# Kernel optimization log

Hardware: AMD Instinct MI355X
Metric: run time of the kernel (lower is better)

## Reference

```python
import jax, jax.numpy as jnp
import numpy as np

IN_C = 256
ATTN_C = IN_C // 8
B, H, W = 4, 64, 64


def setup_inputs() -> dict:
    key = jax.random.key(0)
    ks = jax.random.split(key, 8)
    x = jax.random.normal(ks[0], (B, IN_C, W, H), dtype=jnp.float32)
    # 1x1 convs == channel-mixing matmuls: weight [out_c, in_c], bias [out_c]
    sq = 1.0 / np.sqrt(IN_C)
    Wq = jax.random.normal(ks[1], (ATTN_C, IN_C), dtype=jnp.float32) * sq
    bq = jnp.zeros((ATTN_C,), dtype=jnp.float32)
    Wk = jax.random.normal(ks[2], (ATTN_C, IN_C), dtype=jnp.float32) * sq
    bk = jnp.zeros((ATTN_C,), dtype=jnp.float32)
    Wv = jax.random.normal(ks[3], (IN_C, IN_C), dtype=jnp.float32) * sq
    bv = jnp.zeros((IN_C,), dtype=jnp.float32)
    # gamma initialized to zeros in the torch module; use a nonzero value so
    # the attention path contributes to the output/gradients.
    gamma = jnp.full((1,), 0.5, dtype=jnp.float32)
    return {"x": x, "Wq": Wq, "bq": bq, "Wk": Wk, "bk": bk,
            "Wv": Wv, "bv": bv, "gamma": gamma}


def reference(x, Wq, bq, Wk, bk, Wv, bv, gamma):
    bs, c, w, h = x.shape
    n = w * h
    xf = x.reshape(bs, c, n)                                   # [B, C, N]
    q = jnp.einsum('ac,bcn->ban', Wq, xf) + bq[:, None]        # [B, A, N]
    k = jnp.einsum('ac,bcn->ban', Wk, xf) + bk[:, None]        # [B, A, N]
    v = jnp.einsum('oc,bcn->bon', Wv, xf) + bv[:, None]        # [B, C, N]
    # energy = query.transpose(1,2) @ key  -> energy[b,i,j] = sum_a q[b,a,i] k[b,a,j]
    energy = jnp.einsum('bai,baj->bij', q, k)                  # [B, N, N]
    # non-standard: softmax over dim=1 (the query/i axis)
    attn = jax.nn.softmax(energy, axis=1)
    # out = value @ attn.transpose(1,2) -> out[b,c,i] = sum_j v[b,c,j] attn[b,i,j]
    out = jnp.einsum('bcj,bij->bci', v, attn)                  # [B, C, N]
    out = out.reshape(bs, c, w, h)
    return gamma * out + x
```

## Files before the change

### kernel.cpp

```cpp
#include <hip/hip_runtime.h>

#define NBATCH 4
#define CIN 256
#define CATT 32
#define NPIX 4096

static constexpr float LOG2E_F = 1.4426950408889634f;

typedef __attribute__((ext_vector_type(8))) short bf16x8;
typedef __attribute__((ext_vector_type(4))) float f32x4;

__device__ __forceinline__ unsigned short f2bf_rne(float f) {
    unsigned u = __builtin_bit_cast(unsigned, f);
    return (unsigned short)((u + 0x7fffu + ((u >> 16) & 1u)) >> 16);
}
__device__ __forceinline__ float bf2f(unsigned short h) {
    unsigned u = (unsigned)h << 16;
    return __builtin_bit_cast(float, u);
}
__device__ __forceinline__ void split8(const float* p, bf16x8& hi, bf16x8& lo) {
    const float4 a = *reinterpret_cast<const float4*>(p);
    const float4 b = *reinterpret_cast<const float4*>(p + 4);
    const float f[8] = {a.x, a.y, a.z, a.w, b.x, b.y, b.z, b.w};
    #pragma unroll
    for (int e = 0; e < 8; ++e) {
        const unsigned short h = f2bf_rne(f[e]);
        hi[e] = (short)h;
        lo[e] = (short)f2bf_rne(f[e] - bf2f(h));
    }
}
__device__ __forceinline__ bf16x8 cvt8(const float* p) {
    const float4 a = *reinterpret_cast<const float4*>(p);
    const float4 b = *reinterpret_cast<const float4*>(p + 4);
    const float f[8] = {a.x, a.y, a.z, a.w, b.x, b.y, b.z, b.w};
    bf16x8 r;
    #pragma unroll
    for (int e = 0; e < 8; ++e) r[e] = (short)f2bf_rne(f[e]);
    return r;
}

__global__ __launch_bounds__(256, 2)
void transpose_kernel(const float* __restrict__ x, unsigned short* __restrict__ xT)
{
    __shared__ unsigned short sT[64][68];
    const int t = threadIdx.x;
    const int nblk = blockIdx.x * 64;
    const int cblk = blockIdx.y * 64;
    const int b = blockIdx.z;
    const float* xb = x + ((size_t)b * CIN + cblk) * NPIX + nblk;
    const int lc = t >> 2, ln = (t & 3) << 4;
    #pragma unroll
    for (int u = 0; u < 4; ++u) {
        const float4 v = *reinterpret_cast<const float4*>(&xb[(size_t)lc * NPIX + ln + 4 * u]);
        sT[ln + 4 * u + 0][lc] = f2bf_rne(v.x);
        sT[ln + 4 * u + 1][lc] = f2bf_rne(v.y);
        sT[ln + 4 * u + 2][lc] = f2bf_rne(v.z);
        sT[ln + 4 * u + 3][lc] = f2bf_rne(v.w);
    }
    __syncthreads();
    const int rn = t >> 2, cs = (t & 3) << 4;
    const uint2 d0 = *reinterpret_cast<const uint2*>(&sT[rn][cs + 0]);
    const uint2 d1 = *reinterpret_cast<const uint2*>(&sT[rn][cs + 4]);
    const uint2 d2 = *reinterpret_cast<const uint2*>(&sT[rn][cs + 8]);
    const uint2 d3 = *reinterpret_cast<const uint2*>(&sT[rn][cs + 12]);
    unsigned short* dst = xT + ((size_t)b * NPIX + nblk + rn) * CIN + cblk + cs;
    *reinterpret_cast<uint4*>(dst)     = make_uint4(d0.x, d0.y, d1.x, d1.y);
    *reinterpret_cast<uint4*>(dst + 8) = make_uint4(d2.x, d2.y, d3.x, d3.y);
}

__global__ __launch_bounds__(256, 2)
void proj_qk_kernel(const float* __restrict__ Wq, const float* __restrict__ bq,
                    const float* __restrict__ Wk, const float* __restrict__ bk,
                    const unsigned short* __restrict__ xT,
                    unsigned short* __restrict__ qt, unsigned short* __restrict__ kt)
{
    const int t = threadIdx.x, w = t >> 6, l = t & 63, lr = l & 15, lg = l >> 4;
    const int b = blockIdx.y;
    const int n0 = blockIdx.x * 64 + 16 * w;
    const unsigned short* xrow = xT + ((size_t)b * NPIX + n0 + lr) * CIN + lg * 8;
    f32x4 aq[2] = {{0.f,0.f,0.f,0.f},{0.f,0.f,0.f,0.f}};
    f32x4 ak2[2] = {{0.f,0.f,0.f,0.f},{0.f,0.f,0.f,0.f}};
    #pragma unroll
    for (int ks = 0; ks < 8; ++ks) {
        const int ko = ks * 32 + lg * 8;
        const bf16x8 bx = *reinterpret_cast<const bf16x8*>(xrow + ks * 32);
        #pragma unroll
        for (int mt = 0; mt < 2; ++mt) {
            bf16x8 wh, wl;
            split8(&Wq[(size_t)(mt * 16 + lr) * CIN + ko], wh, wl);
            aq[mt] = __builtin_amdgcn_mfma_f32_16x16x32_bf16(wh, bx, aq[mt], 0, 0, 0);
            aq[mt] = __builtin_amdgcn_mfma_f32_16x16x32_bf16(wl, bx, aq[mt], 0, 0, 0);
            split8(&Wk[(size_t)(mt * 16 + lr) * CIN + ko], wh, wl);
            ak2[mt] = __builtin_amdgcn_mfma_f32_16x16x32_bf16(wh, bx, ak2[mt], 0, 0, 0);
            ak2[mt] = __builtin_amdgcn_mfma_f32_16x16x32_bf16(wl, bx, ak2[mt], 0, 0, 0);
        }
    }
    #pragma unroll
    for (int mt = 0; mt < 2; ++mt) {
        const float4 b4q = *reinterpret_cast<const float4*>(&bq[16 * mt + (lg << 2)]);
        const float4 b4k = *reinterpret_cast<const float4*>(&bk[16 * mt + (lg << 2)]);
        ushort4 uq, uk;
        uq.x = f2bf_rne(LOG2E_F * (aq[mt][0] + b4q.x));
        uq.y = f2bf_rne(LOG2E_F * (aq[mt][1] + b4q.y));
        uq.z = f2bf_rne(LOG2E_F * (aq[mt][2] + b4q.z));
        uq.w = f2bf_rne(LOG2E_F * (aq[mt][3] + b4q.w));
        uk.x = f2bf_rne(ak2[mt][0] + b4k.x);
        uk.y = f2bf_rne(ak2[mt][1] + b4k.y);
        uk.z = f2bf_rne(ak2[mt][2] + b4k.z);
        uk.w = f2bf_rne(ak2[mt][3] + b4k.w);
        const size_t base = ((size_t)b * NPIX + n0 + lr) * CATT + 16 * mt + (lg << 2);
        *reinterpret_cast<ushort4*>(&qt[base]) = uq;
        *reinterpret_cast<ushort4*>(&kt[base]) = uk;
    }
}

__global__ __launch_bounds__(256, 2)
void stats_kernel(const unsigned short* __restrict__ qt,
                  const unsigned short* __restrict__ kt, float* __restrict__ rs)
{
    __shared__ float sred[4][16];
    const int n = blockIdx.x;
    const int b = n & 3;
    const int jblk = (n >> 2) * 32;
    const int t = threadIdx.x, w = t >> 6, l = t & 63, lr = l & 15, lg = l >> 4;
    const int jsl = w & 1;
    const int ih = w >> 1;
    const unsigned short* qb = qt + (size_t)b * NPIX * CATT;
    const unsigned short* kb = kt + (size_t)b * NPIX * CATT;

    const bf16x8 kfrag = *reinterpret_cast<const bf16x8*>(
        &kb[(size_t)(jblk + 16 * jsl + lr) * CATT + lg * 8]);
    const f32x4 zero = {0.f, 0.f, 0.f, 0.f};
    const unsigned short* qp = qb + (size_t)(ih * 2048 + lr) * CATT + lg * 8;

    float s0 = 0.f, s1 = 0.f, s2 = 0.f, s3 = 0.f;
    bf16x8 qc0 = *reinterpret_cast<const bf16x8*>(qp);
    bf16x8 qc1 = *reinterpret_cast<const bf16x8*>(qp + 16 * CATT);
    bf16x8 qc2 = *reinterpret_cast<const bf16x8*>(qp + 32 * CATT);
    bf16x8 qc3 = *reinterpret_cast<const bf16x8*>(qp + 48 * CATT);

    for (int ib = 0; ib < 2048; ib += 64) {
        bf16x8 qn0, qn1, qn2, qn3;
        const bool more = (ib + 64) < 2048;
        if (more) {
            const unsigned short* q2 = qp + (size_t)(ib + 64) * CATT;
            qn0 = *reinterpret_cast<const bf16x8*>(q2);
            qn1 = *reinterpret_cast<const bf16x8*>(q2 + 16 * CATT);
            qn2 = *reinterpret_cast<const bf16x8*>(q2 + 32 * CATT);
            qn3 = *reinterpret_cast<const bf16x8*>(q2 + 48 * CATT);
        }
        f32x4 d;
        d = __builtin_amdgcn_mfma_f32_16x16x32_bf16(kfrag, qc0, zero, 0, 0, 0);
        s0 += __builtin_amdgcn_exp2f(d[0]); s1 += __builtin_amdgcn_exp2f(d[1]);
        s2 += __builtin_amdgcn_exp2f(d[2]); s3 += __builtin_amdgcn_exp2f(d[3]);
        d = __builtin_amdgcn_mfma_f32_16x16x32_bf16(kfrag, qc1, zero, 0, 0, 0);
        s0 += __builtin_amdgcn_exp2f(d[0]); s1 += __builtin_amdgcn_exp2f(d[1]);
        s2 += __builtin_amdgcn_exp2f(d[2]); s3 += __builtin_amdgcn_exp2f(d[3]);
        d = __builtin_amdgcn_mfma_f32_16x16x32_bf16(kfrag, qc2, zero, 0, 0, 0);
        s0 += __builtin_amdgcn_exp2f(d[0]); s1 += __builtin_amdgcn_exp2f(d[1]);
        s2 += __builtin_amdgcn_exp2f(d[2]); s3 += __builtin_amdgcn_exp2f(d[3]);
        d = __builtin_amdgcn_mfma_f32_16x16x32_bf16(kfrag, qc3, zero, 0, 0, 0);
        s0 += __builtin_amdgcn_exp2f(d[0]); s1 += __builtin_amdgcn_exp2f(d[1]);
        s2 += __builtin_amdgcn_exp2f(d[2]); s3 += __builtin_amdgcn_exp2f(d[3]);
        if (more) { qc0 = qn0; qc1 = qn1; qc2 = qn2; qc3 = qn3; }
    }
    #pragma unroll
    for (int m = 1; m < 16; m <<= 1) {
        s0 += __shfl_xor(s0, m); s1 += __shfl_xor(s1, m);
        s2 += __shfl_xor(s2, m); s3 += __shfl_xor(s3, m);
    }
    if (lr == 0) {
        sred[w][(lg << 2) + 0] = s0;
        sred[w][(lg << 2) + 1] = s1;
        sred[w][(lg << 2) + 2] = s2;
        sred[w][(lg << 2) + 3] = s3;
    }
    __syncthreads();
    if (t < 32) {
        const int j16 = t & 15, js = t >> 4;
        const float s = sred[js][j16] + sred[js + 2][j16];
        rs[(size_t)b * NPIX + jblk + t] = 1.0f / s;
    }
}

__global__ __launch_bounds__(256, 2)
void proj_v_kernel(const float* __restrict__ Wv, const float* __restrict__ bv,
                   const unsigned short* __restrict__ xT, const float* __restrict__ rs,
                   const float* __restrict__ gamma, unsigned short* __restrict__ vt)
{
    const int t = threadIdx.x, w = t >> 6, l = t & 63, lr = l & 15, lg = l >> 4;
    const int b = blockIdx.y;
    const int n0 = blockIdx.x * 32;
    const int cb = 64 * w;
    const unsigned short* xa = xT + ((size_t)b * NPIX + n0) * CIN;
    f32x4 acc[2][4] = {};
    #pragma unroll
    for (int ks = 0; ks < 8; ++ks) {
        const int ko = ks * 32 + lg * 8;
        bf16x8 af[2];
        #pragma unroll
        for (int mt = 0; mt < 2; ++mt)
            af[mt] = *reinterpret_cast<const bf16x8*>(&xa[(size_t)(16 * mt + lr) * CIN + ko]);
        #pragma unroll
        for (int ct = 0; ct < 4; ++ct) {
            const bf16x8 wf = cvt8(&Wv[(size_t)(cb + 16 * ct + lr) * CIN + ko]);
            #pragma unroll
            for (int mt = 0; mt < 2; ++mt)
                acc[mt][ct] = __builtin_amdgcn_mfma_f32_16x16x32_bf16(af[mt], wf, acc[mt][ct], 0, 0, 0);
        }
    }
    const float gv = gamma[0];
    #pragma unroll
    for (int mt = 0; mt < 2; ++mt) {
        const int nr = n0 + 16 * mt + (lg << 2);
        const float4 rs4 = *reinterpret_cast<const float4*>(&rs[(size_t)b * NPIX + nr]);
        #pragma unroll
        for (int ct = 0; ct < 4; ++ct) {
            const int c = cb + 16 * ct + lr;
            const float bb = bv[c];
            ushort4 u;
            u.x = f2bf_rne(gv * rs4.x * (acc[mt][ct][0] + bb));
            u.y = f2bf_rne(gv * rs4.y * (acc[mt][ct][1] + bb));
            u.z = f2bf_rne(gv * rs4.z * (acc[mt][ct][2] + bb));
            u.w = f2bf_rne(gv * rs4.w * (acc[mt][ct][3] + bb));
            *reinterpret_cast<ushort4*>(&vt[((size_t)b * CIN + c) * NPIX + nr]) = u;
        }
    }
}

__global__ __launch_bounds__(256, 2)
void out_kernel(const unsigned short* __restrict__ qt,
                const unsigned short* __restrict__ kt,
                const unsigned short* __restrict__ vt,
                const float* __restrict__ x, float* __restrict__ out)
{
    __shared__ unsigned short sP[2][64 * 64];
    const int n = blockIdx.x;
    const int b = n & 3;
    const int rest = n >> 2;
    const int ch = rest & 1;
    const int it = rest >> 1;
    const int iblk = it * 64;
    const int cblk = ch * 128;
    const int t = threadIdx.x, w = t >> 6, l = t & 63, lr = l & 15, lg = l >> 4;
    const unsigned short* qb = qt + (size_t)b * NPIX * CATT;
    const unsigned short* kb = kt + (size_t)b * NPIX * CATT;
    const unsigned short* vb = vt + (size_t)b * CIN * NPIX;
    const f32x4 zero = {0.f, 0.f, 0.f, 0.f};

    bf16x8 qfrag[4];
    #pragma unroll
    for (int nt = 0; nt < 4; ++nt)
        qfrag[nt] = *reinterpret_cast<const bf16x8*>(
            &qb[(size_t)(iblk + 16 * nt + lr) * CATT + lg * 8]);

    const unsigned short* kp = kb + (size_t)(16 * w + lr) * CATT + lg * 8;
    const unsigned short* vp = vb + (size_t)(cblk + 32 * w + lr) * NPIX + lg * 8;

    const int swz = (lr & 7) << 4;
    const int wb0 = lr * 128 + (((16 * w + 4 * lg) * 2) ^ swz);
    const int rb_col0 = (16 * lg) ^ swz;
    const int rb_col1 = (64 + 16 * lg) ^ swz;

    f32x4 acc[2][4] = {};

    const bf16x8 kf0 = *reinterpret_cast<const bf16x8*>(kp);
    bf16x8 vc00 = *reinterpret_cast<const bf16x8*>(vp);
    bf16x8 vc01 = *reinterpret_cast<const bf16x8*>(vp + 32);
    bf16x8 vc10 = *reinterpret_cast<const bf16x8*>(vp + 16 * (size_t)NPIX);
    bf16x8 vc11 = *reinterpret_cast<const bf16x8*>(vp + 16 * (size_t)NPIX + 32);
    bf16x8 kfA  = *reinterpret_cast<const bf16x8*>(kp + (size_t)64 * CATT);
    bf16x8 vn00 = *reinterpret_cast<const bf16x8*>(vp + 64);
    bf16x8 vn01 = *reinterpret_cast<const bf16x8*>(vp + 64 + 32);
    bf16x8 vn10 = *reinterpret_cast<const bf16x8*>(vp + 16 * (size_t)NPIX + 64);
    bf16x8 vn11 = *reinterpret_cast<const bf16x8*>(vp + 16 * (size_t)NPIX + 64 + 32);
    {
        char* spw = reinterpret_cast<char*>(&sP[0][0]);
        #pragma unroll
        for (int nt = 0; nt < 4; ++nt) {
            const f32x4 e = __builtin_amdgcn_mfma_f32_16x16x32_bf16(kf0, qfrag[nt], zero, 0, 0, 0);
            const float p0 = __builtin_amdgcn_exp2f(e[0]);
            const float p1 = __builtin_amdgcn_exp2f(e[1]);
            const float p2 = __builtin_amdgcn_exp2f(e[2]);
            const float p3 = __builtin_amdgcn_exp2f(e[3]);
            unsigned w0, w1;
            asm("v_cvt_pk_bf16_f32 %0, %1, %2" : "=v"(w0) : "v"(p0), "v"(p1));
            asm("v_cvt_pk_bf16_f32 %0, %1, %2" : "=v"(w1) : "v"(p2), "v"(p3));
            *reinterpret_cast<uint2*>(spw + wb0 + nt * 2048) = make_uint2(w0, w1);
        }
    }
    __syncthreads();

    for (int jb = 0; jb < 63; ++jb) {
        const int jpre = (jb + 2 < 64) ? jb + 2 : 63;
        const bf16x8 kfN  = *reinterpret_cast<const bf16x8*>(kp + (size_t)jpre * 64 * CATT);
        const unsigned short* vpp = vp + (size_t)jpre * 64;
        const bf16x8 vN00 = *reinterpret_cast<const bf16x8*>(vpp);
        const bf16x8 vN01 = *reinterpret_cast<const bf16x8*>(vpp + 32);
        const bf16x8 vN10 = *reinterpret_cast<const bf16x8*>(vpp + 16 * (size_t)NPIX);
        const bf16x8 vN11 = *reinterpret_cast<const bf16x8*>(vpp + 16 * (size_t)NPIX + 32);

        char* spw = reinterpret_cast<char*>(&sP[(jb + 1) & 1][0]);
        char* spr = reinterpret_cast<char*>(&sP[jb & 1][0]);

        f32x4 e[4];
        #pragma unroll
        for (int nt = 0; nt < 4; ++nt)
            e[nt] = __builtin_amdgcn_mfma_f32_16x16x32_bf16(kfA, qfrag[nt], zero, 0, 0, 0);

        bf16x8 pf[4];
        #pragma unroll
        for (int nt = 0; nt < 4; ++nt)
            pf[nt] = *reinterpret_cast<const bf16x8*>(spr + lr * 128 + nt * 2048 + rb_col0);
        __builtin_amdgcn_s_setprio(1);
        #pragma unroll
        for (int nt = 0; nt < 4; ++nt) {
            acc[0][nt] = __builtin_amdgcn_mfma_f32_16x16x32_bf16(vc00, pf[nt], acc[0][nt], 0, 0, 0);
            acc[1][nt] = __builtin_amdgcn_mfma_f32_16x16x32_bf16(vc10, pf[nt], acc[1][nt], 0, 0, 0);
        }
        __builtin_amdgcn_s_setprio(0);
        #pragma unroll
        for (int h = 0; h < 2; ++h) {
            const float p0 = __builtin_amdgcn_exp2f(e[h][0]);
            const float p1 = __builtin_amdgcn_exp2f(e[h][1]);
            const float p2 = __builtin_amdgcn_exp2f(e[h][2]);
            const float p3 = __builtin_amdgcn_exp2f(e[h][3]);
            unsigned w0, w1;
            asm("v_cvt_pk_bf16_f32 %0, %1, %2" : "=v"(w0) : "v"(p0), "v"(p1));
            asm("v_cvt_pk_bf16_f32 %0, %1, %2" : "=v"(w1) : "v"(p2), "v"(p3));
            *reinterpret_cast<uint2*>(spw + wb0 + h * 2048) = make_uint2(w0, w1);
        }
        #pragma unroll
        for (int nt = 0; nt < 4; ++nt)
            pf[nt] = *reinterpret_cast<const bf16x8*>(spr + lr * 128 + nt * 2048 + rb_col1);
        __builtin_amdgcn_s_setprio(1);
        #pragma unroll
        for (int nt = 0; nt < 4; ++nt) {
            acc[0][nt] = __builtin_amdgcn_mfma_f32_16x16x32_bf16(vc01, pf[nt], acc[0][nt], 0, 0, 0);
            acc[1][nt] = __builtin_amdgcn_mfma_f32_16x16x32_bf16(vc11, pf[nt], acc[1][nt], 0, 0, 0);
        }
        __builtin_amdgcn_s_setprio(0);
        #pragma unroll
        for (int h = 2; h < 4; ++h) {
            const float p0 = __builtin_amdgcn_exp2f(e[h][0]);
            const float p1 = __builtin_amdgcn_exp2f(e[h][1]);
            const float p2 = __builtin_amdgcn_exp2f(e[h][2]);
            const float p3 = __builtin_amdgcn_exp2f(e[h][3]);
            unsigned w0, w1;
            asm("v_cvt_pk_bf16_f32 %0, %1, %2" : "=v"(w0) : "v"(p0), "v"(p1));
            asm("v_cvt_pk_bf16_f32 %0, %1, %2" : "=v"(w1) : "v"(p2), "v"(p3));
            *reinterpret_cast<uint2*>(spw + wb0 + h * 2048) = make_uint2(w0, w1);
        }
        __syncthreads();
        kfA = kfN;
        vc00 = vn00; vc01 = vn01; vc10 = vn10; vc11 = vn11;
        vn00 = vN00; vn01 = vN01; vn10 = vN10; vn11 = vN11;
    }

    {
        char* spr = reinterpret_cast<char*>(&sP[1][0]);
        bf16x8 pf[4];
        #pragma unroll
        for (int nt = 0; nt < 4; ++nt)
            pf[nt] = *reinterpret_cast<const bf16x8*>(spr + lr * 128 + nt * 2048 + rb_col0);
        #pragma unroll
        for (int nt = 0; nt < 4; ++nt) {
            acc[0][nt] = __builtin_amdgcn_mfma_f32_16x16x32_bf16(vc00, pf[nt], acc[0][nt], 0, 0, 0);
            acc[1][nt] = __builtin_amdgcn_mfma_f32_16x16x32_bf16(vc10, pf[nt], acc[1][nt], 0, 0, 0);
        }
        #pragma unroll
        for (int nt = 0; nt < 4; ++nt)
            pf[nt] = *reinterpret_cast<const bf16x8*>(spr + lr * 128 + nt * 2048 + rb_col1);
        #pragma unroll
        for (int nt = 0; nt < 4; ++nt) {
            acc[0][nt] = __builtin_amdgcn_mfma_f32_16x16x32_bf16(vc01, pf[nt], acc[0][nt], 0, 0, 0);
            acc[1][nt] = __builtin_amdgcn_mfma_f32_16x16x32_bf16(vc11, pf[nt], acc[1][nt], 0, 0, 0);
        }
    }

    const float* xb = x + (size_t)b * CIN * NPIX;
    float* ob = out + (size_t)b * CIN * NPIX;
    #pragma unroll
    for (int mt = 0; mt < 2; ++mt)
        #pragma unroll
        for (int nt = 0; nt < 4; ++nt)
            #pragma unroll
            for (int r = 0; r < 4; ++r) {
                const int c = cblk + 32 * w + 16 * mt + (lg << 2) + r;
                const size_t idx = (size_t)c * NPIX + iblk + 16 * nt + lr;
                ob[idx] = acc[mt][nt][r] + xb[idx];
            }
}

extern "C" void kernel_launch(void* const* d_in, const int* in_sizes, int n_in,
                              void* d_out, int out_size, void* d_ws, size_t ws_size,
                              hipStream_t stream)
{
    const float* x     = (const float*)d_in[0];
    const float* Wq    = (const float*)d_in[1];
    const float* bq    = (const float*)d_in[2];
    const float* Wk    = (const float*)d_in[3];
    const float* bk    = (const float*)d_in[4];
    const float* Wv    = (const float*)d_in[5];
    const float* bv    = (const float*)d_in[6];
    const float* gamma = (const float*)d_in[7];
    float* out = (float*)d_out;

    unsigned short* xT = (unsigned short*)d_ws;
    unsigned short* qt = xT + (size_t)NBATCH * NPIX * CIN;
    unsigned short* kt = qt + (size_t)NBATCH * NPIX * CATT;
    unsigned short* vt = kt + (size_t)NBATCH * NPIX * CATT;
    float* rsw = (float*)(vt + (size_t)NBATCH * CIN * NPIX);

    transpose_kernel<<<dim3(NPIX / 64, CIN / 64, NBATCH), 256, 0, stream>>>(x, xT);
    proj_qk_kernel<<<dim3(NPIX / 64, NBATCH), 256, 0, stream>>>(Wq, bq, Wk, bk, xT, qt, kt);
    stats_kernel<<<dim3((NPIX / 32) * NBATCH), 256, 0, stream>>>(qt, kt, rsw);
    proj_v_kernel<<<dim3(NPIX / 32, NBATCH), 256, 0, stream>>>(Wv, bv, xT, rsw, gamma, vt);
    out_kernel<<<dim3((NPIX / 64) * 2 * NBATCH), 256, 0, stream>>>(qt, kt, vt, x, out);
}
```

Baseline: 134.2 us.

## Rewrite out_kernel with 32x32 MFMA and register-resident P via permlane32 swap

Replaces the 16x16x32 MFMA out kernel, which passed exponentiated scores through double-buffered LDS with a barrier each step, with a per-wave 32x32x16 MFMA scheme. Each wave computes a 32-query-by-32-key score tile, exponentiates it and repacks it in registers with permlane32_swap as the B operand for the PV MFMAs, removing LDS traffic and per-iteration syncs. The grid is remapped to 512 blocks, each covering 128 pixels and 64 channels. Each wave now computes its own score tiles, so QK^T and exp work is duplicated across the four channel-group blocks. A periodic s_barrier keeps the waves roughly aligned.

```diff
diff --git a/kernel.cpp b/kernel.cpp
--- a/kernel.cpp
+++ b/kernel.cpp
@@ -9,6 +9,9 @@
 
 typedef __attribute__((ext_vector_type(8))) short bf16x8;
 typedef __attribute__((ext_vector_type(4))) float f32x4;
+typedef __attribute__((ext_vector_type(16))) float f32x16;
+typedef __attribute__((ext_vector_type(4))) unsigned u32x4;
+typedef __attribute__((ext_vector_type(2))) unsigned u32x2;
 
 __device__ __forceinline__ unsigned short f2bf_rne(float f) {
     unsigned u = __builtin_bit_cast(unsigned, f);
@@ -234,162 +237,89 @@
                 const unsigned short* __restrict__ vt,
                 const float* __restrict__ x, float* __restrict__ out)
 {
-    __shared__ unsigned short sP[2][64 * 64];
     const int n = blockIdx.x;
     const int b = n & 3;
-    const int rest = n >> 2;
-    const int ch = rest & 1;
-    const int it = rest >> 1;
-    const int iblk = it * 64;
-    const int cblk = ch * 128;
-    const int t = threadIdx.x, w = t >> 6, l = t & 63, lr = l & 15, lg = l >> 4;
+    const int cr = (n >> 2) & 3;
+    const int ib = n >> 4;
+    const int cb = cr * 64;
+    const int t = threadIdx.x, w = t >> 6, l = t & 63;
+    const int lm = l & 31, h = l >> 5;
+    const int i0 = ib * 128 + 32 * w;
     const unsigned short* qb = qt + (size_t)b * NPIX * CATT;
     const unsigned short* kb = kt + (size_t)b * NPIX * CATT;
     const unsigned short* vb = vt + (size_t)b * CIN * NPIX;
-    const f32x4 zero = {0.f, 0.f, 0.f, 0.f};
-
-    bf16x8 qfrag[4];
-    #pragma unroll
-    for (int nt = 0; nt < 4; ++nt)
-        qfrag[nt] = *reinterpret_cast<const bf16x8*>(
-            &qb[(size_t)(iblk + 16 * nt + lr) * CATT + lg * 8]);
-
-    const unsigned short* kp = kb + (size_t)(16 * w + lr) * CATT + lg * 8;
-    const unsigned short* vp = vb + (size_t)(cblk + 32 * w + lr) * NPIX + lg * 8;
-
-    const int swz = (lr & 7) << 4;
-    const int wb0 = lr * 128 + (((16 * w + 4 * lg) * 2) ^ swz);
-    const int rb_col0 = (16 * lg) ^ swz;
-    const int rb_col1 = (64 + 16 * lg) ^ swz;
-
-    f32x4 acc[2][4] = {};
-
-    const bf16x8 kf0 = *reinterpret_cast<const bf16x8*>(kp);
-    bf16x8 vc00 = *reinterpret_cast<const bf16x8*>(vp);
-    bf16x8 vc01 = *reinterpret_cast<const bf16x8*>(vp + 32);
-    bf16x8 vc10 = *reinterpret_cast<const bf16x8*>(vp + 16 * (size_t)NPIX);
-    bf16x8 vc11 = *reinterpret_cast<const bf16x8*>(vp + 16 * (size_t)NPIX + 32);
-    bf16x8 kfA  = *reinterpret_cast<const bf16x8*>(kp + (size_t)64 * CATT);
-    bf16x8 vn00 = *reinterpret_cast<const bf16x8*>(vp + 64);
-    bf16x8 vn01 = *reinterpret_cast<const bf16x8*>(vp + 64 + 32);
-    bf16x8 vn10 = *reinterpret_cast<const bf16x8*>(vp + 16 * (size_t)NPIX + 64);
-    bf16x8 vn11 = *reinterpret_cast<const bf16x8*>(vp + 16 * (size_t)NPIX + 64 + 32);
-    {
-        char* spw = reinterpret_cast<char*>(&sP[0][0]);
-        #pragma unroll
-        for (int nt = 0; nt < 4; ++nt) {
-            const f32x4 e = __builtin_amdgcn_mfma_f32_16x16x32_bf16(kf0, qfrag[nt], zero, 0, 0, 0);
-            const float p0 = __builtin_amdgcn_exp2f(e[0]);
-            const float p1 = __builtin_amdgcn_exp2f(e[1]);
-            const float p2 = __builtin_amdgcn_exp2f(e[2]);
-            const float p3 = __builtin_amdgcn_exp2f(e[3]);
-            unsigned w0, w1;
-            asm("v_cvt_pk_bf16_f32 %0, %1, %2" : "=v"(w0) : "v"(p0), "v"(p1));
-            asm("v_cvt_pk_bf16_f32 %0, %1, %2" : "=v"(w1) : "v"(p2), "v"(p3));
-            *reinterpret_cast<uint2*>(spw + wb0 + nt * 2048) = make_uint2(w0, w1);
-        }
-    }
-    __syncthreads();
-
-    for (int jb = 0; jb < 63; ++jb) {
-        const int jpre = (jb + 2 < 64) ? jb + 2 : 63;
-        const bf16x8 kfN  = *reinterpret_cast<const bf16x8*>(kp + (size_t)jpre * 64 * CATT);
-        const unsigned short* vpp = vp + (size_t)jpre * 64;
-        const bf16x8 vN00 = *reinterpret_cast<const bf16x8*>(vpp);
-        const bf16x8 vN01 = *reinterpret_cast<const bf16x8*>(vpp + 32);
-        const bf16x8 vN10 = *reinterpret_cast<const bf16x8*>(vpp + 16 * (size_t)NPIX);
-        const bf16x8 vN11 = *reinterpret_cast<const bf16x8*>(vpp + 16 * (size_t)NPIX + 32);
-
-        char* spw = reinterpret_cast<char*>(&sP[(jb + 1) & 1][0]);
-        char* spr = reinterpret_cast<char*>(&sP[jb & 1][0]);
-
-        f32x4 e[4];
-        #pragma unroll
-        for (int nt = 0; nt < 4; ++nt)
-            e[nt] = __builtin_amdgcn_mfma_f32_16x16x32_bf16(kfA, qfrag[nt], zero, 0, 0, 0);
-
-        bf16x8 pf[4];
-        #pragma unroll
-        for (int nt = 0; nt < 4; ++nt)
-            pf[nt] = *reinterpret_cast<const bf16x8*>(spr + lr * 128 + nt * 2048 + rb_col0);
-        __builtin_amdgcn_s_setprio(1);
-        #pragma unroll
-        for (int nt = 0; nt < 4; ++nt) {
-            acc[0][nt] = __builtin_amdgcn_mfma_f32_16x16x32_bf16(vc00, pf[nt], acc[0][nt], 0, 0, 0);
-            acc[1][nt] = __builtin_amdgcn_mfma_f32_16x16x32_bf16(vc10, pf[nt], acc[1][nt], 0, 0, 0);
-        }
-        __builtin_amdgcn_s_setprio(0);
-        #pragma unroll
-        for (int h = 0; h < 2; ++h) {
-            const float p0 = __builtin_amdgcn_exp2f(e[h][0]);
-            const float p1 = __builtin_amdgcn_exp2f(e[h][1]);
-            const float p2 = __builtin_amdgcn_exp2f(e[h][2]);
-            const float p3 = __builtin_amdgcn_exp2f(e[h][3]);
-            unsigned w0, w1;
-            asm("v_cvt_pk_bf16_f32 %0, %1, %2" : "=v"(w0) : "v"(p0), "v"(p1));
-            asm("v_cvt_pk_bf16_f32 %0, %1, %2" : "=v"(w1) : "v"(p2), "v"(p3));
-            *reinterpret_cast<uint2*>(spw + wb0 + h * 2048) = make_uint2(w0, w1);
-        }
-        #pragma unroll
-        for (int nt = 0; nt < 4; ++nt)
-            pf[nt] = *reinterpret_cast<const bf16x8*>(spr + lr * 128 + nt * 2048 + rb_col1);
-        __builtin_amdgcn_s_setprio(1);
-        #pragma unroll
-        for (int nt = 0; nt < 4; ++nt) {
-            acc[0][nt] = __builtin_amdgcn_mfma_f32_16x16x32_bf16(vc01, pf[nt], acc[0][nt], 0, 0, 0);
-            acc[1][nt] = __builtin_amdgcn_mfma_f32_16x16x32_bf16(vc11, pf[nt], acc[1][nt], 0, 0, 0);
-        }
-        __builtin_amdgcn_s_setprio(0);
-        #pragma unroll
-        for (int h = 2; h < 4; ++h) {
-            const float p0 = __builtin_amdgcn_exp2f(e[h][0]);
-            const float p1 = __builtin_amdgcn_exp2f(e[h][1]);
-            const float p2 = __builtin_amdgcn_exp2f(e[h][2]);
-            const float p3 = __builtin_amdgcn_exp2f(e[h][3]);
-            unsigned w0, w1;
-            asm("v_cvt_pk_bf16_f32 %0, %1, %2" : "=v"(w0) : "v"(p0), "v"(p1));
-            asm("v_cvt_pk_bf16_f32 %0, %1, %2" : "=v"(w1) : "v"(p2), "v"(p3));
-            *reinterpret_cast<uint2*>(spw + wb0 + h * 2048) = make_uint2(w0, w1);
-        }
-        __syncthreads();
-        kfA = kfN;
-        vc00 = vn00; vc01 = vn01; vc10 = vn10; vc11 = vn11;
-        vn00 = vN00; vn01 = vN01; vn10 = vN10; vn11 = vN11;
-    }
-
-    {
-        char* spr = reinterpret_cast<char*>(&sP[1][0]);
-        bf16x8 pf[4];
-        #pragma unroll
-        for (int nt = 0; nt < 4; ++nt)
-            pf[nt] = *reinterpret_cast<const bf16x8*>(spr + lr * 128 + nt * 2048 + rb_col0);
-        #pragma unroll
-        for (int nt = 0; nt < 4; ++nt) {
-            acc[0][nt] = __builtin_amdgcn_mfma_f32_16x16x32_bf16(vc00, pf[nt], acc[0][nt], 0, 0, 0);
-            acc[1][nt] = __builtin_amdgcn_mfma_f32_16x16x32_bf16(vc10, pf[nt], acc[1][nt], 0, 0, 0);
-        }
-        #pragma unroll
-        for (int nt = 0; nt < 4; ++nt)
-            pf[nt] = *reinterpret_cast<const bf16x8*>(spr + lr * 128 + nt * 2048 + rb_col1);
-        #pragma unroll
-        for (int nt = 0; nt < 4; ++nt) {
-            acc[0][nt] = __builtin_amdgcn_mfma_f32_16x16x32_bf16(vc01, pf[nt], acc[0][nt], 0, 0, 0);
-            acc[1][nt] = __builtin_amdgcn_mfma_f32_16x16x32_bf16(vc11, pf[nt], acc[1][nt], 0, 0, 0);
-        }
+
+    const unsigned short* qp = qb + (size_t)(i0 + lm) * CATT + 8 * h;
+    const bf16x8 qf0 = *reinterpret_cast<const bf16x8*>(qp);
+    const bf16x8 qf1 = *reinterpret_cast<const bf16x8*>(qp + 16);
+
+    const unsigned short* kp  = kb + (size_t)lm * CATT + 8 * h;
+    const unsigned short* vp0 = vb + (size_t)(cb + lm) * NPIX + 8 * h;
+    const unsigned short* vp1 = vp0 + (size_t)32 * NPIX;
+
+    f32x16 acc0 = {};
+    f32x16 acc1 = {};
+    const f32x16 zero16 = {};
+
+    bf16x8 kc0 = *reinterpret_cast<const bf16x8*>(kp);
+    bf16x8 kc1 = *reinterpret_cast<const bf16x8*>(kp + 16);
+    bf16x8 v00 = *reinterpret_cast<const bf16x8*>(vp0);
+    bf16x8 v01 = *reinterpret_cast<const bf16x8*>(vp0 + 16);
+    bf16x8 v10 = *reinterpret_cast<const bf16x8*>(vp1);
+    bf16x8 v11 = *reinterpret_cast<const bf16x8*>(vp1 + 16);
+
+    for (int jb = 0; jb < 128; ++jb) {
+        bf16x8 kn0, kn1, w00, w01, w10, w11;
+        const bool more = jb < 127;
+        if (more) {
+            const int jn = (jb + 1) * 32;
+            const unsigned short* kq = kp + (size_t)jn * CATT;
+            kn0 = *reinterpret_cast<const bf16x8*>(kq);
+            kn1 = *reinterpret_cast<const bf16x8*>(kq + 16);
+            w00 = *reinterpret_cast<const bf16x8*>(vp0 + jn);
+            w01 = *reinterpret_cast<const bf16x8*>(vp0 + jn + 16);
+            w10 = *reinterpret_cast<const bf16x8*>(vp1 + jn);
+            w11 = *reinterpret_cast<const bf16x8*>(vp1 + jn + 16);
+        }
+        f32x16 d = __builtin_amdgcn_mfma_f32_32x32x16_bf16(kc0, qf0, zero16, 0, 0, 0);
+        d = __builtin_amdgcn_mfma_f32_32x32x16_bf16(kc1, qf1, d, 0, 0, 0);
+        float p[16];
+        #pragma unroll
+        for (int r = 0; r < 16; ++r) p[r] = __builtin_amdgcn_exp2f(d[r]);
+        unsigned c01, c23, c45, c67, c89, cAB, cCD, cEF;
+        asm("v_cvt_pk_bf16_f32 %0, %1, %2" : "=v"(c01) : "v"(p[0]),  "v"(p[1]));
+        asm("v_cvt_pk_bf16_f32 %0, %1, %2" : "=v"(c23) : "v"(p[2]),  "v"(p[3]));
+        asm("v_cvt_pk_bf16_f32 %0, %1, %2" : "=v"(c45) : "v"(p[4]),  "v"(p[5]));
+        asm("v_cvt_pk_bf16_f32 %0, %1, %2" : "=v"(c67) : "v"(p[6]),  "v"(p[7]));
+        asm("v_cvt_pk_bf16_f32 %0, %1, %2" : "=v"(c89) : "v"(p[8]),  "v"(p[9]));
+        asm("v_cvt_pk_bf16_f32 %0, %1, %2" : "=v"(cAB) : "v"(p[10]), "v"(p[11]));
+        asm("v_cvt_pk_bf16_f32 %0, %1, %2" : "=v"(cCD) : "v"(p[12]), "v"(p[13]));
+        asm("v_cvt_pk_bf16_f32 %0, %1, %2" : "=v"(cEF) : "v"(p[14]), "v"(p[15]));
+        u32x2 s;
+        s = __builtin_amdgcn_permlane32_swap(c01, c45, false, false); c01 = s[0]; c45 = s[1];
+        s = __builtin_amdgcn_permlane32_swap(c23, c67, false, false); c23 = s[0]; c67 = s[1];
+        s = __builtin_amdgcn_permlane32_swap(c89, cCD, false, false); c89 = s[0]; cCD = s[1];
+        s = __builtin_amdgcn_permlane32_swap(cAB, cEF, false, false); cAB = s[0]; cEF = s[1];
+        const bf16x8 B0 = __builtin_bit_cast(bf16x8, (u32x4){c01, c23, c45, c67});
+        const bf16x8 B1 = __builtin_bit_cast(bf16x8, (u32x4){c89, cAB, cCD, cEF});
+        acc0 = __builtin_amdgcn_mfma_f32_32x32x16_bf16(v00, B0, acc0, 0, 0, 0);
+        acc0 = __builtin_amdgcn_mfma_f32_32x32x16_bf16(v01, B1, acc0, 0, 0, 0);
+        acc1 = __builtin_amdgcn_mfma_f32_32x32x16_bf16(v10, B0, acc1, 0, 0, 0);
+        acc1 = __builtin_amdgcn_mfma_f32_32x32x16_bf16(v11, B1, acc1, 0, 0, 0);
+        if (more) { kc0 = kn0; kc1 = kn1; v00 = w00; v01 = w01; v10 = w10; v11 = w11; }
+        if ((jb & 15) == 15) __builtin_amdgcn_s_barrier();
     }
 
     const float* xb = x + (size_t)b * CIN * NPIX;
     float* ob = out + (size_t)b * CIN * NPIX;
     #pragma unroll
-    for (int mt = 0; mt < 2; ++mt)
-        #pragma unroll
-        for (int nt = 0; nt < 4; ++nt)
-            #pragma unroll
-            for (int r = 0; r < 4; ++r) {
-                const int c = cblk + 32 * w + 16 * mt + (lg << 2) + r;
-                const size_t idx = (size_t)c * NPIX + iblk + 16 * nt + lr;
-                ob[idx] = acc[mt][nt][r] + xb[idx];
-            }
+    for (int r = 0; r < 16; ++r) {
+        const int crow = (r & 3) + 8 * (r >> 2) + 4 * h;
+        const size_t idx0 = (size_t)(cb + crow) * NPIX + i0 + lm;
+        ob[idx0] = acc0[r] + xb[idx0];
+        const size_t idx1 = idx0 + (size_t)32 * NPIX;
+        ob[idx1] = acc1[r] + xb[idx1];
+    }
 }
 
 extern "C" void kernel_launch(void* const* d_in, const int* in_sizes, int n_in,
@@ -416,5 +346,5 @@
     proj_qk_kernel<<<dim3(NPIX / 64, NBATCH), 256, 0, stream>>>(Wq, bq, Wk, bk, xT, qt, kt);
     stats_kernel<<<dim3((NPIX / 32) * NBATCH), 256, 0, stream>>>(qt, kt, rsw);
     proj_v_kernel<<<dim3(NPIX / 32, NBATCH), 256, 0, stream>>>(Wv, bv, xT, rsw, gamma, vt);
-    out_kernel<<<dim3((NPIX / 64) * 2 * NBATCH), 256, 0, stream>>>(qt, kt, vt, x, out);
-}
+    out_kernel<<<dim3(512), 256, 0, stream>>>(qt, kt, vt, x, out);
+}
```

Result: slower. 207.5 us (+54.6%).

## Stage V and K tiles through LDS with async global_load_lds triple buffering

Applied to the files above, without the earlier changes.

Replaces the register-prefetched V and K fragment loads in out_kernel with direct global-to-LDS async copies into swizzled shared buffers: V is triple-buffered, K and P are double-buffered. The loop is restructured so each iteration computes P for the current block while consuming P and V from the previous block, with one barrier per iteration. The aim is to cut VGPR pressure and hide global latency behind the DMA path. In exchange, LDS use grows to about 64 KB per block, which may limit the two-blocks-per-CU occupancy, and it adds LDS read traffic.

```diff
diff --git a/kernel.cpp b/kernel.cpp
--- a/kernel.cpp
+++ b/kernel.cpp
@@ -37,6 +37,11 @@
     #pragma unroll
     for (int e = 0; e < 8; ++e) r[e] = (short)f2bf_rne(f[e]);
     return r;
+}
+__device__ __forceinline__ void gl_lds16(const unsigned short* g, unsigned short* l) {
+    __builtin_amdgcn_global_load_lds(
+        (const __attribute__((address_space(1))) unsigned int*)g,
+        (__attribute__((address_space(3))) unsigned int*)l, 16, 0, 0);
 }
 
 __global__ __launch_bounds__(256, 2)
@@ -234,7 +239,9 @@
                 const unsigned short* __restrict__ vt,
                 const float* __restrict__ x, float* __restrict__ out)
 {
-    __shared__ unsigned short sP[2][64 * 64];
+    __shared__ unsigned short sV[3][128 * 64];
+    __shared__ unsigned short sK[2][64 * 32];
+    __shared__ unsigned short sPl[2][64 * 64];
     const int n = blockIdx.x;
     const int b = n & 3;
     const int rest = n >> 2;
@@ -254,9 +261,26 @@
         qfrag[nt] = *reinterpret_cast<const bf16x8*>(
             &qb[(size_t)(iblk + 16 * nt + lr) * CATT + lg * 8]);
 
-    const unsigned short* kp = kb + (size_t)(16 * w + lr) * CATT + lg * 8;
-    const unsigned short* vp = vb + (size_t)(cblk + 32 * w + lr) * NPIX + lg * 8;
-
+    const unsigned short* vsrcq[4];
+    #pragma unroll
+    for (int q = 0; q < 4; ++q) {
+        const int r = (4 * w + q) * 8 + (l >> 3);
+        const int p = l & 7;
+        vsrcq[q] = vb + (size_t)(cblk + r) * NPIX + ((p ^ (r & 7)) * 8);
+    }
+    const int rk = w * 16 + (l >> 2);
+    const unsigned short* ksrc0 = kb + (size_t)rk * CATT + (((l & 3) ^ (rk & 3)) * 8);
+
+    const int krow = 16 * w + lr;
+    const int kbyte = krow * 64 + ((lg * 16) ^ ((krow & 3) << 4));
+    const int cl0 = 32 * w + lr;
+    const int cl1 = cl0 + 16;
+    int vbyte[2][2];
+    #pragma unroll
+    for (int kk = 0; kk < 2; ++kk) {
+        vbyte[0][kk] = cl0 * 128 + ((kk * 64 + lg * 16) ^ ((cl0 & 7) << 4));
+        vbyte[1][kk] = cl1 * 128 + ((kk * 64 + lg * 16) ^ ((cl1 & 7) << 4));
+    }
     const int swz = (lr & 7) << 4;
     const int wb0 = lr * 128 + (((16 * w + 4 * lg) * 2) ^ swz);
     const int rb_col0 = (16 * lg) ^ swz;
@@ -264,117 +288,81 @@
 
     f32x4 acc[2][4] = {};
 
-    const bf16x8 kf0 = *reinterpret_cast<const bf16x8*>(kp);
-    bf16x8 vc00 = *reinterpret_cast<const bf16x8*>(vp);
-    bf16x8 vc01 = *reinterpret_cast<const bf16x8*>(vp + 32);
-    bf16x8 vc10 = *reinterpret_cast<const bf16x8*>(vp + 16 * (size_t)NPIX);
-    bf16x8 vc11 = *reinterpret_cast<const bf16x8*>(vp + 16 * (size_t)NPIX + 32);
-    bf16x8 kfA  = *reinterpret_cast<const bf16x8*>(kp + (size_t)64 * CATT);
-    bf16x8 vn00 = *reinterpret_cast<const bf16x8*>(vp + 64);
-    bf16x8 vn01 = *reinterpret_cast<const bf16x8*>(vp + 64 + 32);
-    bf16x8 vn10 = *reinterpret_cast<const bf16x8*>(vp + 16 * (size_t)NPIX + 64);
-    bf16x8 vn11 = *reinterpret_cast<const bf16x8*>(vp + 16 * (size_t)NPIX + 64 + 32);
+    #pragma unroll
+    for (int q = 0; q < 4; ++q) gl_lds16(vsrcq[q], &sV[0][(4 * w + q) * 512]);
+    gl_lds16(ksrc0, &sK[0][w * 512]);
+    __syncthreads();
+
+    int vs_cur = 0;
+    for (int jb = 0; jb < 64; ++jb) {
+        const int vs_next = (vs_cur == 2) ? 0 : vs_cur + 1;
+        const int vs_prev = (vs_cur == 0) ? 2 : vs_cur - 1;
+        if (jb < 63) {
+            const int jn = (jb + 1) * 64;
+            #pragma unroll
+            for (int q = 0; q < 4; ++q)
+                gl_lds16(vsrcq[q] + jn, &sV[vs_next][(4 * w + q) * 512]);
+            gl_lds16(ksrc0 + (size_t)jn * CATT, &sK[(jb + 1) & 1][w * 512]);
+        }
+        {
+            const char* skp = reinterpret_cast<const char*>(&sK[jb & 1][0]);
+            const bf16x8 kf = *reinterpret_cast<const bf16x8*>(skp + kbyte);
+            char* spw = reinterpret_cast<char*>(&sPl[jb & 1][0]);
+            #pragma unroll
+            for (int nt = 0; nt < 4; ++nt) {
+                const f32x4 e = __builtin_amdgcn_mfma_f32_16x16x32_bf16(kf, qfrag[nt], zero, 0, 0, 0);
+                const float p0 = __builtin_amdgcn_exp2f(e[0]);
+                const float p1 = __builtin_amdgcn_exp2f(e[1]);
+                const float p2 = __builtin_amdgcn_exp2f(e[2]);
+                const float p3 = __builtin_amdgcn_exp2f(e[3]);
+                unsigned w0, w1;
+                asm("v_cvt_pk_bf16_f32 %0, %1, %2" : "=v"(w0) : "v"(p0), "v"(p1));
+                asm("v_cvt_pk_bf16_f32 %0, %1, %2" : "=v"(w1) : "v"(p2), "v"(p3));
+                *reinterpret_cast<uint2*>(spw + wb0 + nt * 2048) = make_uint2(w0, w1);
+            }
+        }
+        if (jb > 0) {
+            const char* spr = reinterpret_cast<const char*>(&sPl[(jb - 1) & 1][0]);
+            const char* svp = reinterpret_cast<const char*>(&sV[vs_prev][0]);
+            #pragma unroll
+            for (int kk = 0; kk < 2; ++kk) {
+                const int rbc = (kk == 0) ? rb_col0 : rb_col1;
+                bf16x8 pf[4];
+                #pragma unroll
+                for (int nt = 0; nt < 4; ++nt)
+                    pf[nt] = *reinterpret_cast<const bf16x8*>(spr + lr * 128 + nt * 2048 + rbc);
+                const bf16x8 v0 = *reinterpret_cast<const bf16x8*>(svp + vbyte[0][kk]);
+                const bf16x8 v1 = *reinterpret_cast<const bf16x8*>(svp + vbyte[1][kk]);
+                __builtin_amdgcn_s_setprio(1);
+                #pragma unroll
+                for (int nt = 0; nt < 4; ++nt) {
+                    acc[0][nt] = __builtin_amdgcn_mfma_f32_16x16x32_bf16(v0, pf[nt], acc[0][nt], 0, 0, 0);
+                    acc[1][nt] = __builtin_amdgcn_mfma_f32_16x16x32_bf16(v1, pf[nt], acc[1][nt], 0, 0, 0);
+                }
+                __builtin_amdgcn_s_setprio(0);
+            }
+        }
+        __syncthreads();
+        vs_cur = vs_next;
+    }
     {
-        char* spw = reinterpret_cast<char*>(&sP[0][0]);
-        #pragma unroll
-        for (int nt = 0; nt < 4; ++nt) {
-            const f32x4 e = __builtin_amdgcn_mfma_f32_16x16x32_bf16(kf0, qfrag[nt], zero, 0, 0, 0);
-            const float p0 = __builtin_amdgcn_exp2f(e[0]);
-            const float p1 = __builtin_amdgcn_exp2f(e[1]);
-            const float p2 = __builtin_amdgcn_exp2f(e[2]);
-            const float p3 = __builtin_amdgcn_exp2f(e[3]);
-            unsigned w0, w1;
-            asm("v_cvt_pk_bf16_f32 %0, %1, %2" : "=v"(w0) : "v"(p0), "v"(p1));
-            asm("v_cvt_pk_bf16_f32 %0, %1, %2" : "=v"(w1) : "v"(p2), "v"(p3));
-            *reinterpret_cast<uint2*>(spw + wb0 + nt * 2048) = make_uint2(w0, w1);
-        }
-    }
-    __syncthreads();
-
-    for (int jb = 0; jb < 63; ++jb) {
-        const int jpre = (jb + 2 < 64) ? jb + 2 : 63;
-        const bf16x8 kfN  = *reinterpret_cast<const bf16x8*>(kp + (size_t)jpre * 64 * CATT);
-        const unsigned short* vpp = vp + (size_t)jpre * 64;
-        const bf16x8 vN00 = *reinterpret_cast<const bf16x8*>(vpp);
-        const bf16x8 vN01 = *reinterpret_cast<const bf16x8*>(vpp + 32);
-        const bf16x8 vN10 = *reinterpret_cast<const bf16x8*>(vpp + 16 * (size_t)NPIX);
-        const bf16x8 vN11 = *reinterpret_cast<const bf16x8*>(vpp + 16 * (size_t)NPIX + 32);
-
-        char* spw = reinterpret_cast<char*>(&sP[(jb + 1) & 1][0]);
-        char* spr = reinterpret_cast<char*>(&sP[jb & 1][0]);
-
-        f32x4 e[4];
-        #pragma unroll
-        for (int nt = 0; nt < 4; ++nt)
-            e[nt] = __builtin_amdgcn_mfma_f32_16x16x32_bf16(kfA, qfrag[nt], zero, 0, 0, 0);
-
-        bf16x8 pf[4];
-        #pragma unroll
-        for (int nt = 0; nt < 4; ++nt)
-            pf[nt] = *reinterpret_cast<const bf16x8*>(spr + lr * 128 + nt * 2048 + rb_col0);
-        __builtin_amdgcn_s_setprio(1);
-        #pragma unroll
-        for (int nt = 0; nt < 4; ++nt) {
-            acc[0][nt] = __builtin_amdgcn_mfma_f32_16x16x32_bf16(vc00, pf[nt], acc[0][nt], 0, 0, 0);
-            acc[1][nt] = __builtin_amdgcn_mfma_f32_16x16x32_bf16(vc10, pf[nt], acc[1][nt], 0, 0, 0);
-        }
-        __builtin_amdgcn_s_setprio(0);
-        #pragma unroll
-        for (int h = 0; h < 2; ++h) {
-            const float p0 = __builtin_amdgcn_exp2f(e[h][0]);
-            const float p1 = __builtin_amdgcn_exp2f(e[h][1]);
-            const float p2 = __builtin_amdgcn_exp2f(e[h][2]);
-            const float p3 = __builtin_amdgcn_exp2f(e[h][3]);
-            unsigned w0, w1;
-            asm("v_cvt_pk_bf16_f32 %0, %1, %2" : "=v"(w0) : "v"(p0), "v"(p1));
-            asm("v_cvt_pk_bf16_f32 %0, %1, %2" : "=v"(w1) : "v"(p2), "v"(p3));
-            *reinterpret_cast<uint2*>(spw + wb0 + h * 2048) = make_uint2(w0, w1);
-        }
-        #pragma unroll
-        for (int nt = 0; nt < 4; ++nt)
-            pf[nt] = *reinterpret_cast<const bf16x8*>(spr + lr * 128 + nt * 2048 + rb_col1);
-        __builtin_amdgcn_s_setprio(1);
-        #pragma unroll
-        for (int nt = 0; nt < 4; ++nt) {
-            acc[0][nt] = __builtin_amdgcn_mfma_f32_16x16x32_bf16(vc01, pf[nt], acc[0][nt], 0, 0, 0);
-            acc[1][nt] = __builtin_amdgcn_mfma_f32_16x16x32_bf16(vc11, pf[nt], acc[1][nt], 0, 0, 0);
-        }
-        __builtin_amdgcn_s_setprio(0);
-        #pragma unroll
-        for (int h = 2; h < 4; ++h) {
-            const float p0 = __builtin_amdgcn_exp2f(e[h][0]);
-            const float p1 = __builtin_amdgcn_exp2f(e[h][1]);
-            const float p2 = __builtin_amdgcn_exp2f(e[h][2]);
-            const float p3 = __builtin_amdgcn_exp2f(e[h][3]);
-            unsigned w0, w1;
-            asm("v_cvt_pk_bf16_f32 %0, %1, %2" : "=v"(w0) : "v"(p0), "v"(p1));
-            asm("v_cvt_pk_bf16_f32 %0, %1, %2" : "=v"(w1) : "v"(p2), "v"(p3));
-            *reinterpret_cast<uint2*>(spw + wb0 + h * 2048) = make_uint2(w0, w1);
-        }
-        __syncthreads();
-        kfA = kfN;
-        vc00 = vn00; vc01 = vn01; vc10 = vn10; vc11 = vn11;
-        vn00 = vN00; vn01 = vN01; vn10 = vN10; vn11 = vN11;
-    }
-
-    {
-        char* spr = reinterpret_cast<char*>(&sP[1][0]);
-        bf16x8 pf[4];
-        #pragma unroll
-        for (int nt = 0; nt < 4; ++nt)
-            pf[nt] = *reinterpret_cast<const bf16x8*>(spr + lr * 128 + nt * 2048 + rb_col0);
-        #pragma unroll
-        for (int nt = 0; nt < 4; ++nt) {
-            acc[0][nt] = __builtin_amdgcn_mfma_f32_16x16x32_bf16(vc00, pf[nt], acc[0][nt], 0, 0, 0);
-            acc[1][nt] = __builtin_amdgcn_mfma_f32_16x16x32_bf16(vc10, pf[nt], acc[1][nt], 0, 0, 0);
-        }
-        #pragma unroll
-        for (int nt = 0; nt < 4; ++nt)
-            pf[nt] = *reinterpret_cast<const bf16x8*>(spr + lr * 128 + nt * 2048 + rb_col1);
-        #pragma unroll
-        for (int nt = 0; nt < 4; ++nt) {
-            acc[0][nt] = __builtin_amdgcn_mfma_f32_16x16x32_bf16(vc01, pf[nt], acc[0][nt], 0, 0, 0);
-            acc[1][nt] = __builtin_amdgcn_mfma_f32_16x16x32_bf16(vc11, pf[nt], acc[1][nt], 0, 0, 0);
+        const int vs_prev = (vs_cur == 0) ? 2 : vs_cur - 1;
+        const char* spr = reinterpret_cast<const char*>(&sPl[1][0]);
+        const char* svp = reinterpret_cast<const char*>(&sV[vs_prev][0]);
+        #pragma unroll
+        for (int kk = 0; kk < 2; ++kk) {
+            const int rbc = (kk == 0) ? rb_col0 : rb_col1;
+            bf16x8 pf[4];
+            #pragma unroll
+            for (int nt = 0; nt < 4; ++nt)
+                pf[nt] = *reinterpret_cast<const bf16x8*>(spr + lr * 128 + nt * 2048 + rbc);
+            const bf16x8 v0 = *reinterpret_cast<const bf16x8*>(svp + vbyte[0][kk]);
+            const bf16x8 v1 = *reinterpret_cast<const bf16x8*>(svp + vbyte[1][kk]);
+            #pragma unroll
+            for (int nt = 0; nt < 4; ++nt) {
+                acc[0][nt] = __builtin_amdgcn_mfma_f32_16x16x32_bf16(v0, pf[nt], acc[0][nt], 0, 0, 0);
+                acc[1][nt] = __builtin_amdgcn_mfma_f32_16x16x32_bf16(v1, pf[nt], acc[1][nt], 0, 0, 0);
+            }
         }
     }
 
```

New measurement: 128.3 us (median of 2 runs). -4.4%, faster.
